# Kernel optimization log

Hardware: AMD Instinct MI355X
Metric: run time of the kernel (lower is better)

Reference implementation:

```python
import jax, jax.numpy as jnp
import numpy as np

N_DIM = 32
N_HEADS = 4
HEAD_SIZE = N_DIM // N_HEADS  # 8


def setup_inputs() -> dict:
    key = jax.random.key(0)
    ks = jax.random.split(key, 9)
    B, T = 16, 2048
    s = 1.0 / np.sqrt(N_DIM)
    inp = {
        "x": jax.random.normal(ks[0], (B, T, N_DIM), dtype=jnp.float32),
        "Wq": jax.random.uniform(ks[1], (N_DIM, N_DIM), jnp.float32, -s, s),
        "bq": jax.random.uniform(ks[2], (N_DIM,), jnp.float32, -s, s),
        "Wk": jax.random.uniform(ks[3], (N_DIM, N_DIM), jnp.float32, -s, s),
        "bk": jax.random.uniform(ks[4], (N_DIM,), jnp.float32, -s, s),
        "Wv": jax.random.uniform(ks[5], (N_DIM, N_DIM), jnp.float32, -s, s),
        "bv": jax.random.uniform(ks[6], (N_DIM,), jnp.float32, -s, s),
        "Wp": jax.random.uniform(ks[7], (N_DIM, N_DIM), jnp.float32, -s, s),
        "bp": jax.random.uniform(ks[8], (N_DIM,), jnp.float32, -s, s),
    }
    return inp


def reference(x, Wq, bq, Wk, bk, Wv, bv, Wp, bp):
    b, t, c = x.shape
    # nn.Linear: y = x @ W^T + b
    def heads(W, bias):
        y = jnp.einsum("btc,dc->btd", x, W) + bias
        return y.reshape(b, t, N_HEADS, HEAD_SIZE).transpose(0, 2, 1, 3)  # [b,h,t,d]

    q = heads(Wq, bq)
    k = heads(Wk, bk)
    v = heads(Wv, bv)

    scores = jnp.einsum("bhqd,bhkd->bhqk", q, k) / np.sqrt(HEAD_SIZE)  # [b,h,t,t]
    causal = jnp.tril(jnp.ones((t, t), dtype=bool))
    scores = jnp.where(causal[None, None], scores, -jnp.inf)
    weights = jax.nn.softmax(scores, axis=-1)
    # dropout layers are identity in eval mode
    z = jnp.einsum("bhqk,bhkd->bhqd", weights, v)
    z = z.transpose(0, 2, 1, 3).reshape(b, t, N_DIM)
    z = jnp.einsum("btc,dc->btd", z, Wp) + bp
    return z
```

## Files before the change

### kernel.cpp

```cpp
#include <hip/hip_runtime.h>
#include <math.h>

#define BB 16
#define TT 2048
#define CC 32
#define HH 4
#define DD 8

typedef __fp16 h2  __attribute__((ext_vector_type(2)));
typedef __fp16 h8  __attribute__((ext_vector_type(8)));
typedef float  fx16 __attribute__((ext_vector_type(16)));
typedef int    i4v __attribute__((ext_vector_type(4)));

__device__ __forceinline__ h2 pkh(float a, float b) {
#if __has_builtin(__builtin_amdgcn_cvt_pkrtz)
    return __builtin_amdgcn_cvt_pkrtz(a, b);
#else
    h2 r; r.x = (__fp16)a; r.y = (__fp16)b; return r;
#endif
}

__device__ __forceinline__ float fexp2(float x) {
#if __has_builtin(__builtin_amdgcn_exp2f)
    return __builtin_amdgcn_exp2f(x);
#else
    return exp2f(x);
#endif
}

__device__ __forceinline__ int h2bits(h2 v) { return __builtin_bit_cast(int, v); }

__global__ __launch_bounds__(256) void qkv_kernel(
    const float* __restrict__ x,
    const float* __restrict__ Wq, const float* __restrict__ bq,
    const float* __restrict__ Wk, const float* __restrict__ bk,
    const float* __restrict__ Wv, const float* __restrict__ bv,
    __fp16* __restrict__ Qo, __fp16* __restrict__ Ko, __fp16* __restrict__ Vo)
{
    const int row = blockIdx.x * 256 + threadIdx.x;
    const int m = blockIdx.y >> 2, h = blockIdx.y & 3;
    const int b = row >> 11, t = row & 2047;
    const int bh = b * HH + h;

    const float* W    = (m == 0) ? Wq : (m == 1) ? Wk : Wv;
    const float* bias = (m == 0) ? bq : (m == 1) ? bk : bv;

    float xr[CC];
    const float4* xp = (const float4*)(x + (size_t)row * CC);
    #pragma unroll
    for (int i = 0; i < CC / 4; i++) {
        float4 f = xp[i];
        xr[4*i+0] = f.x; xr[4*i+1] = f.y; xr[4*i+2] = f.z; xr[4*i+3] = f.w;
    }

    float o[DD];
    #pragma unroll
    for (int d = 0; d < DD; d++) {
        const int dd = h * DD + d;
        float acc = bias[dd];
        #pragma unroll
        for (int c = 0; c < CC; c++) acc += xr[c] * W[dd * CC + c];
        o[d] = acc;
    }

    if (m == 0) {
        const float qs = 0.3535533905932738f * 1.4426950408889634f;
        i4v qw;
        qw.x = h2bits(pkh(o[0]*qs, o[1]*qs)); qw.y = h2bits(pkh(o[2]*qs, o[3]*qs));
        qw.z = h2bits(pkh(o[4]*qs, o[5]*qs)); qw.w = h2bits(pkh(o[6]*qs, o[7]*qs));
        *(i4v*)(Qo + ((size_t)bh * TT + t) * DD) = qw;
    } else if (m == 1) {
        i4v kw;
        kw.x = h2bits(pkh(o[0], o[1])); kw.y = h2bits(pkh(o[2], o[3]));
        kw.z = h2bits(pkh(o[4], o[5])); kw.w = h2bits(pkh(o[6], o[7]));
        *(i4v*)(Ko + ((size_t)bh * TT + t) * DD) = kw;
    } else {
        __fp16* vt = Vo + (size_t)bh * 9 * TT + t;
        #pragma unroll
        for (int d = 0; d < DD; d++) vt[d * TT] = (__fp16)o[d];
        vt[8 * TT] = (__fp16)1.0f;
    }
}

__global__ __launch_bounds__(512, 4) void attn_kernel(
    const __fp16* __restrict__ Qg, const __fp16* __restrict__ Kg,
    const __fp16* __restrict__ Vg, float* __restrict__ Z)
{
    __shared__ __align__(16) __fp16 Ks[TT * DD + 8];
    __shared__ __align__(16) __fp16 Vts[9 * TT];

    const int tid  = threadIdx.x;
    const int bh   = blockIdx.x >> 3;
    const int bi   = blockIdx.x & 7;
    const int wave = tid >> 6;
    const int lane = tid & 63;
    const int qc   = lane & 31;
    const int hi   = lane >> 5;

    {
        const i4v* Ksrc = (const i4v*)(Kg + (size_t)bh * TT * DD);
        i4v* Kd = (i4v*)Ks;
        for (int i = tid; i < TT * DD / 8; i += 512) Kd[i] = Ksrc[i];
        const i4v* Vsrc = (const i4v*)(Vg + (size_t)bh * 9 * TT);
        i4v* Vd = (i4v*)Vts;
        for (int i = tid; i < 9 * TT / 8; i += 512) Vd[i] = Vsrc[i];
        if (tid == 0) {
            i4v zz; zz.x = 0; zz.y = 0; zz.z = 0; zz.w = 0;
            Kd[TT * DD / 8] = zz;
        }
    }
    __syncthreads();

    const int j = (wave + bi) & 7;
    const int g = 16 * (j >> 1) + ((j & 1) ? (15 - bi) : bi);
    const int qbase = g * 32;
    const int q = qbase + qc;

    h8 qf;
    {
        h8 ql = *(const h8*)(Qg + ((size_t)bh * TT + q) * DD);
        h8 qz;
        #pragma unroll
        for (int i = 0; i < 8; i++) qz[i] = (__fp16)0.0f;
        qf = hi ? qz : ql;
    }

    fx16 O, zc;
    #pragma unroll
    for (int i = 0; i < 16; i++) { O[i] = 0.0f; zc[i] = 0.0f; }

    const int vrow = (qc < 9) ? qc : 8;
    const __fp16* vbase = Vts + vrow * TT + 8 * hi;
    const __fp16* kptr  = Ks + qc * DD;
    const int thr = qc - 4 * hi;

    for (int kt = 0; kt <= qbase; kt += 32) {
        const bool last = (kt == qbase);

        h8 kf = *(const h8*)(kptr + kt * DD);
        fx16 S = __builtin_amdgcn_mfma_f32_32x32x16_f16(kf, qf, zc, 0, 0, 0);

        float p[16];
        #pragma unroll
        for (int r = 0; r < 16; r++) {
            const int ko = (r & 3) + 8 * (r >> 2);
            float sv = S[r];
            if (last) sv = (ko <= thr) ? sv : -INFINITY;
            p[r] = fexp2(sv);
        }

        int Hh[8];
        #pragma unroll
        for (int i = 0; i < 8; i++) Hh[i] = h2bits(pkh(p[2*i], p[2*i+1]));

        #pragma unroll
        for (int s = 0; s < 2; s++) {
            const int b0 = 4 * s;
            int own0 = hi ? Hh[b0+2] : Hh[b0+0];
            int own1 = hi ? Hh[b0+3] : Hh[b0+1];
            int snd0 = hi ? Hh[b0+0] : Hh[b0+2];
            int snd1 = hi ? Hh[b0+1] : Hh[b0+3];
            int rcv0 = __shfl_xor(snd0, 32);
            int rcv1 = __shfl_xor(snd1, 32);
            i4v f;
            f.x = hi ? rcv0 : own0;
            f.y = hi ? rcv1 : own1;
            f.z = hi ? own0 : rcv0;
            f.w = hi ? own1 : rcv1;
            h8 P = __builtin_bit_cast(h8, f);
            h8 vf = *(const h8*)(vbase + kt + 16 * s);
            O = __builtin_amdgcn_mfma_f32_32x32x16_f16(vf, P, O, 0, 0, 0);
        }
    }

    const float inv = 1.0f / O[4];
    const int b = bh >> 2, h = bh & 3;
    float* z = Z + ((size_t)b * TT + q) * CC + h * DD + 4 * hi;
    *(float4*)z = make_float4(O[0]*inv, O[1]*inv, O[2]*inv, O[3]*inv);
}

__global__ __launch_bounds__(256) void proj_kernel(
    const float* __restrict__ Zw, const float* __restrict__ Wp,
    const float* __restrict__ bp, float* __restrict__ out)
{
    const int row = blockIdx.x * 256 + threadIdx.x;
    const int oc = blockIdx.y;

    float zr[CC];
    const float4* zp = (const float4*)(Zw + (size_t)row * CC);
    #pragma unroll
    for (int i = 0; i < CC / 4; i++) {
        float4 f = zp[i];
        zr[4*i+0] = f.x; zr[4*i+1] = f.y; zr[4*i+2] = f.z; zr[4*i+3] = f.w;
    }

    float o[DD];
    #pragma unroll
    for (int d = 0; d < DD; d++) {
        const int dd = oc * DD + d;
        float acc = bp[dd];
        #pragma unroll
        for (int c = 0; c < CC; c++) acc += zr[c] * Wp[dd * CC + c];
        o[d] = acc;
    }

    float* dst = out + (size_t)row * CC + oc * DD;
    ((float4*)dst)[0] = make_float4(o[0], o[1], o[2], o[3]);
    ((float4*)dst)[1] = make_float4(o[4], o[5], o[6], o[7]);
}

extern "C" void kernel_launch(void* const* d_in, const int* in_sizes, int n_in,
                              void* d_out, int out_size, void* d_ws, size_t ws_size,
                              hipStream_t stream) {
    const float* x  = (const float*)d_in[0];
    const float* Wq = (const float*)d_in[1];
    const float* bq = (const float*)d_in[2];
    const float* Wk = (const float*)d_in[3];
    const float* bk = (const float*)d_in[4];
    const float* Wv = (const float*)d_in[5];
    const float* bv = (const float*)d_in[6];
    const float* Wp = (const float*)d_in[7];
    const float* bp = (const float*)d_in[8];
    float* out = (float*)d_out;

    const size_t NE = (size_t)BB * HH * TT * DD;
    __fp16* Qh = (__fp16*)d_ws;
    __fp16* Kh = Qh + NE;
    __fp16* Vt = Kh + NE;
    float*  Zw = (float*)(Vt + (size_t)BB * HH * 9 * TT);

    qkv_kernel<<<dim3(BB * TT / 256, 12), 256, 0, stream>>>(x, Wq, bq, Wk, bk, Wv, bv, Qh, Kh, Vt);
    attn_kernel<<<dim3(BB * HH * 8), 512, 0, stream>>>(Qh, Kh, Vt, Zw);
    proj_kernel<<<dim3(BB * TT / 256, 4), 256, 0, stream>>>(Zw, Wp, bp, out);
}
```

Before: 119.7 us.

## Fuse output projection into attention and restructure blocks across heads with streamed K/V tiles

The attention kernel now assigns each block 64 query rows of one batch across all four heads. It streams K/V in 256-key chunks through padded shared memory instead of loading each head's full K/V. The output projection is fused in through a shared-memory Z buffer, which removes the separate proj kernel and the Z round trip through global memory. The QKV kernel stages x through shared memory and loops over heads per block, which cuts redundant x reads. In exchange there are many more __syncthreads, and waves idle through chunks beyond their causal range. Load imbalance across blocks also changes.

Result: slower. 130.0 us (+8.6%).

```diff
diff --git a/kernel.cpp b/kernel.cpp
--- a/kernel.cpp
+++ b/kernel.cpp
@@ -6,6 +6,11 @@
 #define CC 32
 #define HH 4
 #define DD 8
+
+#define KP 2056
+#define VP 264
+#define VHP (9 * VP)
+#define ZP 33
 
 typedef __fp16 h2  __attribute__((ext_vector_type(2)));
 typedef __fp16 h8  __attribute__((ext_vector_type(8)));
@@ -37,84 +42,88 @@
     const float* __restrict__ Wv, const float* __restrict__ bv,
     __fp16* __restrict__ Qo, __fp16* __restrict__ Ko, __fp16* __restrict__ Vo)
 {
-    const int row = blockIdx.x * 256 + threadIdx.x;
-    const int m = blockIdx.y >> 2, h = blockIdx.y & 3;
+    __shared__ float Xs[256 * ZP];
+    const int tid = threadIdx.x;
+    const int m = blockIdx.y;
+    const int row0 = blockIdx.x * 256;
+
+    {
+        const float4* xg = (const float4*)(x + (size_t)row0 * CC);
+        #pragma unroll
+        for (int i = 0; i < 8; i++) {
+            const int idx = tid + 256 * i;
+            float4 f = xg[idx];
+            const int w = idx * 4;
+            float* d = &Xs[(w >> 5) * ZP + (w & 31)];
+            d[0] = f.x; d[1] = f.y; d[2] = f.z; d[3] = f.w;
+        }
+    }
+    __syncthreads();
+
+    const int row = row0 + tid;
     const int b = row >> 11, t = row & 2047;
-    const int bh = b * HH + h;
+
+    float xr[CC];
+    #pragma unroll
+    for (int c = 0; c < CC; c++) xr[c] = Xs[tid * ZP + c];
 
     const float* W    = (m == 0) ? Wq : (m == 1) ? Wk : Wv;
     const float* bias = (m == 0) ? bq : (m == 1) ? bk : bv;
 
-    float xr[CC];
-    const float4* xp = (const float4*)(x + (size_t)row * CC);
-    #pragma unroll
-    for (int i = 0; i < CC / 4; i++) {
-        float4 f = xp[i];
-        xr[4*i+0] = f.x; xr[4*i+1] = f.y; xr[4*i+2] = f.z; xr[4*i+3] = f.w;
-    }
-
-    float o[DD];
-    #pragma unroll
-    for (int d = 0; d < DD; d++) {
-        const int dd = h * DD + d;
-        float acc = bias[dd];
-        #pragma unroll
-        for (int c = 0; c < CC; c++) acc += xr[c] * W[dd * CC + c];
-        o[d] = acc;
-    }
-
-    if (m == 0) {
-        const float qs = 0.3535533905932738f * 1.4426950408889634f;
-        i4v qw;
-        qw.x = h2bits(pkh(o[0]*qs, o[1]*qs)); qw.y = h2bits(pkh(o[2]*qs, o[3]*qs));
-        qw.z = h2bits(pkh(o[4]*qs, o[5]*qs)); qw.w = h2bits(pkh(o[6]*qs, o[7]*qs));
-        *(i4v*)(Qo + ((size_t)bh * TT + t) * DD) = qw;
-    } else if (m == 1) {
-        i4v kw;
-        kw.x = h2bits(pkh(o[0], o[1])); kw.y = h2bits(pkh(o[2], o[3]));
-        kw.z = h2bits(pkh(o[4], o[5])); kw.w = h2bits(pkh(o[6], o[7]));
-        *(i4v*)(Ko + ((size_t)bh * TT + t) * DD) = kw;
-    } else {
-        __fp16* vt = Vo + (size_t)bh * 9 * TT + t;
-        #pragma unroll
-        for (int d = 0; d < DD; d++) vt[d * TT] = (__fp16)o[d];
-        vt[8 * TT] = (__fp16)1.0f;
+    for (int h = 0; h < HH; h++) {
+        const int bh = b * HH + h;
+        float o[DD];
+        #pragma unroll
+        for (int d = 0; d < DD; d++) {
+            const int dd = h * DD + d;
+            float acc = bias[dd];
+            #pragma unroll
+            for (int c = 0; c < CC; c++) acc += xr[c] * W[dd * CC + c];
+            o[d] = acc;
+        }
+        if (m == 0) {
+            const float qs = 0.3535533905932738f * 1.4426950408889634f;
+            i4v qw;
+            qw.x = h2bits(pkh(o[0]*qs, o[1]*qs)); qw.y = h2bits(pkh(o[2]*qs, o[3]*qs));
+            qw.z = h2bits(pkh(o[4]*qs, o[5]*qs)); qw.w = h2bits(pkh(o[6]*qs, o[7]*qs));
+            *(i4v*)(Qo + ((size_t)bh * TT + t) * DD) = qw;
+        } else if (m == 1) {
+            i4v kw;
+            kw.x = h2bits(pkh(o[0], o[1])); kw.y = h2bits(pkh(o[2], o[3]));
+            kw.z = h2bits(pkh(o[4], o[5])); kw.w = h2bits(pkh(o[6], o[7]));
+            *(i4v*)(Ko + ((size_t)bh * TT + t) * DD) = kw;
+        } else {
+            __fp16* vt = Vo + (size_t)bh * 9 * TT + t;
+            #pragma unroll
+            for (int d = 0; d < DD; d++) vt[d * TT] = (__fp16)o[d];
+            vt[8 * TT] = (__fp16)1.0f;
+        }
     }
 }
 
 __global__ __launch_bounds__(512, 4) void attn_kernel(
     const __fp16* __restrict__ Qg, const __fp16* __restrict__ Kg,
-    const __fp16* __restrict__ Vg, float* __restrict__ Z)
+    const __fp16* __restrict__ Vg,
+    const float* __restrict__ Wp, const float* __restrict__ bp,
+    float* __restrict__ out)
 {
-    __shared__ __align__(16) __fp16 Ks[TT * DD + 8];
-    __shared__ __align__(16) __fp16 Vts[9 * TT];
-
-    const int tid  = threadIdx.x;
-    const int bh   = blockIdx.x >> 3;
-    const int bi   = blockIdx.x & 7;
-    const int wave = tid >> 6;
-    const int lane = tid & 63;
-    const int qc   = lane & 31;
-    const int hi   = lane >> 5;
-
-    {
-        const i4v* Ksrc = (const i4v*)(Kg + (size_t)bh * TT * DD);
-        i4v* Kd = (i4v*)Ks;
-        for (int i = tid; i < TT * DD / 8; i += 512) Kd[i] = Ksrc[i];
-        const i4v* Vsrc = (const i4v*)(Vg + (size_t)bh * 9 * TT);
-        i4v* Vd = (i4v*)Vts;
-        for (int i = tid; i < 9 * TT / 8; i += 512) Vd[i] = Vsrc[i];
-        if (tid == 0) {
-            i4v zz; zz.x = 0; zz.y = 0; zz.z = 0; zz.w = 0;
-            Kd[TT * DD / 8] = zz;
-        }
-    }
-    __syncthreads();
-
-    const int j = (wave + bi) & 7;
-    const int g = 16 * (j >> 1) + ((j & 1) ? (15 - bi) : bi);
-    const int qbase = g * 32;
-    const int q = qbase + qc;
+    __shared__ __align__(16) __fp16 KsS[4 * KP];
+    __shared__ __align__(16) __fp16 VtS[4 * VHP];
+    __shared__ float zbuf[64 * ZP];
+
+    const int tid   = threadIdx.x;
+    const int b     = blockIdx.x & 15;
+    const int qg    = 31 - (blockIdx.x >> 4);
+    const int wavei = tid >> 6;
+    const int lane  = tid & 63;
+    const int qc    = lane & 31;
+    const int hi    = lane >> 5;
+    const int h     = wavei & 3;
+    const int p     = wavei >> 2;
+
+    const int bh    = b * HH + h;
+    const int qbase = qg * 64 + p * 32;
+    const int q     = qbase + qc;
 
     h8 qf;
     {
@@ -130,83 +139,100 @@
     for (int i = 0; i < 16; i++) { O[i] = 0.0f; zc[i] = 0.0f; }
 
     const int vrow = (qc < 9) ? qc : 8;
-    const __fp16* vbase = Vts + vrow * TT + 8 * hi;
-    const __fp16* kptr  = Ks + qc * DD;
-    const int thr = qc - 4 * hi;
-
-    for (int kt = 0; kt <= qbase; kt += 32) {
-        const bool last = (kt == qbase);
-
-        h8 kf = *(const h8*)(kptr + kt * DD);
-        fx16 S = __builtin_amdgcn_mfma_f32_32x32x16_f16(kf, qf, zc, 0, 0, 0);
-
-        float p[16];
-        #pragma unroll
-        for (int r = 0; r < 16; r++) {
-            const int ko = (r & 3) + 8 * (r >> 2);
-            float sv = S[r];
-            if (last) sv = (ko <= thr) ? sv : -INFINITY;
-            p[r] = fexp2(sv);
-        }
-
-        int Hh[8];
-        #pragma unroll
-        for (int i = 0; i < 8; i++) Hh[i] = h2bits(pkh(p[2*i], p[2*i+1]));
-
-        #pragma unroll
-        for (int s = 0; s < 2; s++) {
-            const int b0 = 4 * s;
-            int own0 = hi ? Hh[b0+2] : Hh[b0+0];
-            int own1 = hi ? Hh[b0+3] : Hh[b0+1];
-            int snd0 = hi ? Hh[b0+0] : Hh[b0+2];
-            int snd1 = hi ? Hh[b0+1] : Hh[b0+3];
-            int rcv0 = __shfl_xor(snd0, 32);
-            int rcv1 = __shfl_xor(snd1, 32);
-            i4v f;
-            f.x = hi ? rcv0 : own0;
-            f.y = hi ? rcv1 : own1;
-            f.z = hi ? own0 : rcv0;
-            f.w = hi ? own1 : rcv1;
-            h8 P = __builtin_bit_cast(h8, f);
-            h8 vf = *(const h8*)(vbase + kt + 16 * s);
-            O = __builtin_amdgcn_mfma_f32_32x32x16_f16(vf, P, O, 0, 0, 0);
-        }
-    }
-
-    const float inv = 1.0f / O[4];
-    const int b = bh >> 2, h = bh & 3;
-    float* z = Z + ((size_t)b * TT + q) * CC + h * DD + 4 * hi;
-    *(float4*)z = make_float4(O[0]*inv, O[1]*inv, O[2]*inv, O[3]*inv);
-}
-
-__global__ __launch_bounds__(256) void proj_kernel(
-    const float* __restrict__ Zw, const float* __restrict__ Wp,
-    const float* __restrict__ bp, float* __restrict__ out)
-{
-    const int row = blockIdx.x * 256 + threadIdx.x;
-    const int oc = blockIdx.y;
-
-    float zr[CC];
-    const float4* zp = (const float4*)(Zw + (size_t)row * CC);
-    #pragma unroll
-    for (int i = 0; i < CC / 4; i++) {
-        float4 f = zp[i];
-        zr[4*i+0] = f.x; zr[4*i+1] = f.y; zr[4*i+2] = f.z; zr[4*i+3] = f.w;
-    }
-
-    float o[DD];
-    #pragma unroll
-    for (int d = 0; d < DD; d++) {
-        const int dd = oc * DD + d;
-        float acc = bp[dd];
-        #pragma unroll
-        for (int c = 0; c < CC; c++) acc += zr[c] * Wp[dd * CC + c];
-        o[d] = acc;
-    }
-
-    float* dst = out + (size_t)row * CC + oc * DD;
-    ((float4*)dst)[0] = make_float4(o[0], o[1], o[2], o[3]);
-    ((float4*)dst)[1] = make_float4(o[4], o[5], o[6], o[7]);
+    const int thr  = qc - 4 * hi;
+    const int nst  = qg / 4 + 1;
+
+    for (int sti = 0; sti < nst; sti++) {
+        const int st = sti * 256;
+        __syncthreads();
+        {
+            const int hh = tid >> 7, tl = tid & 127;
+            const i4v* ks = (const i4v*)(Kg + ((size_t)(b * HH + hh) * TT + st) * DD);
+            i4v* kd = (i4v*)(KsS + hh * KP);
+            kd[tl]       = ks[tl];
+            kd[tl + 128] = ks[tl + 128];
+            #pragma unroll
+            for (int i0 = 0; i0 < 3; i0++) {
+                const int i = tl + 128 * i0;
+                if (i < 288) {
+                    const int vr = i >> 5, vc = (i & 31) * 8;
+                    *(i4v*)(VtS + hh * VHP + vr * VP + vc) =
+                        *(const i4v*)(Vg + ((size_t)(b * HH + hh) * 9 + vr) * TT + st + vc);
+                }
+            }
+        }
+        __syncthreads();
+
+        if (st > qbase) continue;
+        const int ktend = min(st + 256, qbase + 32);
+        const __fp16* kbase = KsS + h * KP + qc * DD;
+        const __fp16* vb    = VtS + h * VHP + vrow * VP + 8 * hi;
+
+        for (int kt = st; kt < ktend; kt += 32) {
+            const bool last = (kt == qbase);
+
+            h8 kf = *(const h8*)(kbase + (kt - st) * DD);
+            fx16 S = __builtin_amdgcn_mfma_f32_32x32x16_f16(kf, qf, zc, 0, 0, 0);
+
+            float pe[16];
+            #pragma unroll
+            for (int r = 0; r < 16; r++) {
+                const int ko = (r & 3) + 8 * (r >> 2);
+                float sv = S[r];
+                if (last) sv = (ko <= thr) ? sv : -INFINITY;
+                pe[r] = fexp2(sv);
+            }
+
+            int Hh[8];
+            #pragma unroll
+            for (int i = 0; i < 8; i++) Hh[i] = h2bits(pkh(pe[2*i], pe[2*i+1]));
+
+            #pragma unroll
+            for (int s = 0; s < 2; s++) {
+                const int b0 = 4 * s;
+                int own0 = hi ? Hh[b0+2] : Hh[b0+0];
+                int own1 = hi ? Hh[b0+3] : Hh[b0+1];
+                int snd0 = hi ? Hh[b0+0] : Hh[b0+2];
+                int snd1 = hi ? Hh[b0+1] : Hh[b0+3];
+                int rcv0 = __shfl_xor(snd0, 32);
+                int rcv1 = __shfl_xor(snd1, 32);
+                i4v f;
+                f.x = hi ? rcv0 : own0;
+                f.y = hi ? rcv1 : own1;
+                f.z = hi ? own0 : rcv0;
+                f.w = hi ? own1 : rcv1;
+                h8 P = __builtin_bit_cast(h8, f);
+                h8 vf = *(const h8*)(vb + (kt - st) + 16 * s);
+                O = __builtin_amdgcn_mfma_f32_32x32x16_f16(vf, P, O, 0, 0, 0);
+            }
+        }
+    }
+
+    {
+        const float inv = 1.0f / O[4];
+        float* zp_ = &zbuf[(p * 32 + qc) * ZP + h * DD + 4 * hi];
+        zp_[0] = O[0]*inv; zp_[1] = O[1]*inv; zp_[2] = O[2]*inv; zp_[3] = O[3]*inv;
+    }
+    __syncthreads();
+
+    {
+        const int seg = wavei;
+        const int r = lane;
+        float zr_[CC];
+        #pragma unroll
+        for (int c = 0; c < CC; c++) zr_[c] = zbuf[r * ZP + c];
+        float o4[4];
+        #pragma unroll
+        for (int d = 0; d < 4; d++) {
+            const int dd = seg * 4 + d;
+            float acc = bp[dd];
+            #pragma unroll
+            for (int c = 0; c < CC; c++) acc += zr_[c] * Wp[dd * CC + c];
+            o4[d] = acc;
+        }
+        float* dst = out + ((size_t)b * TT + qg * 64 + r) * CC + seg * 4;
+        *(float4*)dst = make_float4(o4[0], o4[1], o4[2], o4[3]);
+    }
 }
 
 extern "C" void kernel_launch(void* const* d_in, const int* in_sizes, int n_in,
@@ -227,9 +253,7 @@
     __fp16* Qh = (__fp16*)d_ws;
     __fp16* Kh = Qh + NE;
     __fp16* Vt = Kh + NE;
-    float*  Zw = (float*)(Vt + (size_t)BB * HH * 9 * TT);
-
-    qkv_kernel<<<dim3(BB * TT / 256, 12), 256, 0, stream>>>(x, Wq, bq, Wk, bk, Wv, bv, Qh, Kh, Vt);
-    attn_kernel<<<dim3(BB * HH * 8), 512, 0, stream>>>(Qh, Kh, Vt, Zw);
-    proj_kernel<<<dim3(BB * TT / 256, 4), 256, 0, stream>>>(Zw, Wp, bp, out);
-}
+
+    qkv_kernel<<<dim3(BB * TT / 256, 3), 256, 0, stream>>>(x, Wq, bq, Wk, bk, Wv, bv, Qh, Kh, Vt);
+    attn_kernel<<<dim3(BB * 32), 512, 0, stream>>>(Qh, Kh, Vt, Wp, bp, out);
+}
```

## Split attention into single-wave blocks streaming K/V chunks; loop heads in QKV

Applied to the files above, without the earlier changes.

The attention kernel now launches one 64-thread block per (query tile, batch-head) pair, 4096 blocks in all, instead of 512-thread blocks that each staged a whole head's K and V in LDS. Each block streams K/V in 256-key chunks through small LDS buffers and orders tiles so the longest causal work is scheduled first. The aim is to cut LDS footprint, raise occupancy and balance load, at the cost of re-reading K/V from global memory once per query tile. The QKV kernel stages x through padded shared memory and loops over the four heads inside each block, reading x once per matrix rather than once per head.

New measurement: 130.4 us. +9.0%, slower.

```diff
diff --git a/kernel.cpp b/kernel.cpp
--- a/kernel.cpp
+++ b/kernel.cpp
@@ -6,6 +6,9 @@
 #define CC 32
 #define HH 4
 #define DD 8
+#define ZP 33
+#define KBS 2056
+#define VRS 264
 
 typedef __fp16 h2  __attribute__((ext_vector_type(2)));
 typedef __fp16 h8  __attribute__((ext_vector_type(8)));
@@ -29,6 +32,36 @@
 }
 
 __device__ __forceinline__ int h2bits(h2 v) { return __builtin_bit_cast(int, v); }
+
+__device__ __forceinline__ void makeP(const fx16& S, bool last, int thr, int hi, h8* P) {
+    float pe[16];
+    #pragma unroll
+    for (int r = 0; r < 16; r++) {
+        const int ko = (r & 3) + 8 * (r >> 2);
+        float sv = S[r];
+        if (last) sv = (ko <= thr) ? sv : -INFINITY;
+        pe[r] = fexp2(sv);
+    }
+    int Hh[8];
+    #pragma unroll
+    for (int i = 0; i < 8; i++) Hh[i] = h2bits(pkh(pe[2*i], pe[2*i+1]));
+    #pragma unroll
+    for (int s = 0; s < 2; s++) {
+        const int b0 = 4 * s;
+        int own0 = hi ? Hh[b0+2] : Hh[b0+0];
+        int own1 = hi ? Hh[b0+3] : Hh[b0+1];
+        int snd0 = hi ? Hh[b0+0] : Hh[b0+2];
+        int snd1 = hi ? Hh[b0+1] : Hh[b0+3];
+        int rcv0 = __shfl_xor(snd0, 32);
+        int rcv1 = __shfl_xor(snd1, 32);
+        i4v f;
+        f.x = hi ? rcv0 : own0;
+        f.y = hi ? rcv1 : own1;
+        f.z = hi ? own0 : rcv0;
+        f.w = hi ? own1 : rcv1;
+        P[s] = __builtin_bit_cast(h8, f);
+    }
+}
 
 __global__ __launch_bounds__(256) void qkv_kernel(
     const float* __restrict__ x,
@@ -37,91 +70,91 @@
     const float* __restrict__ Wv, const float* __restrict__ bv,
     __fp16* __restrict__ Qo, __fp16* __restrict__ Ko, __fp16* __restrict__ Vo)
 {
-    const int row = blockIdx.x * 256 + threadIdx.x;
-    const int m = blockIdx.y >> 2, h = blockIdx.y & 3;
+    __shared__ float Xs[256 * ZP];
+    const int tid = threadIdx.x;
+    const int m = blockIdx.y;
+    const int row0 = blockIdx.x * 256;
+
+    {
+        const float4* xg = (const float4*)(x + (size_t)row0 * CC);
+        #pragma unroll
+        for (int i = 0; i < 8; i++) {
+            const int idx = tid + 256 * i;
+            float4 f = xg[idx];
+            const int w = idx * 4;
+            float* d = &Xs[(w >> 5) * ZP + (w & 31)];
+            d[0] = f.x; d[1] = f.y; d[2] = f.z; d[3] = f.w;
+        }
+    }
+    __syncthreads();
+
+    const int row = row0 + tid;
     const int b = row >> 11, t = row & 2047;
-    const int bh = b * HH + h;
+
+    float xr[CC];
+    #pragma unroll
+    for (int c = 0; c < CC; c++) xr[c] = Xs[tid * ZP + c];
 
     const float* W    = (m == 0) ? Wq : (m == 1) ? Wk : Wv;
     const float* bias = (m == 0) ? bq : (m == 1) ? bk : bv;
 
-    float xr[CC];
-    const float4* xp = (const float4*)(x + (size_t)row * CC);
-    #pragma unroll
-    for (int i = 0; i < CC / 4; i++) {
-        float4 f = xp[i];
-        xr[4*i+0] = f.x; xr[4*i+1] = f.y; xr[4*i+2] = f.z; xr[4*i+3] = f.w;
-    }
-
-    float o[DD];
-    #pragma unroll
-    for (int d = 0; d < DD; d++) {
-        const int dd = h * DD + d;
-        float acc = bias[dd];
-        #pragma unroll
-        for (int c = 0; c < CC; c++) acc += xr[c] * W[dd * CC + c];
-        o[d] = acc;
-    }
-
-    if (m == 0) {
-        const float qs = 0.3535533905932738f * 1.4426950408889634f;
-        i4v qw;
-        qw.x = h2bits(pkh(o[0]*qs, o[1]*qs)); qw.y = h2bits(pkh(o[2]*qs, o[3]*qs));
-        qw.z = h2bits(pkh(o[4]*qs, o[5]*qs)); qw.w = h2bits(pkh(o[6]*qs, o[7]*qs));
-        *(i4v*)(Qo + ((size_t)bh * TT + t) * DD) = qw;
-    } else if (m == 1) {
-        i4v kw;
-        kw.x = h2bits(pkh(o[0], o[1])); kw.y = h2bits(pkh(o[2], o[3]));
-        kw.z = h2bits(pkh(o[4], o[5])); kw.w = h2bits(pkh(o[6], o[7]));
-        *(i4v*)(Ko + ((size_t)bh * TT + t) * DD) = kw;
-    } else {
-        __fp16* vt = Vo + (size_t)bh * 9 * TT + t;
-        #pragma unroll
-        for (int d = 0; d < DD; d++) vt[d * TT] = (__fp16)o[d];
-        vt[8 * TT] = (__fp16)1.0f;
-    }
-}
-
-__global__ __launch_bounds__(512, 4) void attn_kernel(
+    for (int h = 0; h < HH; h++) {
+        const int bh = b * HH + h;
+        float o[DD];
+        #pragma unroll
+        for (int d = 0; d < DD; d++) {
+            const int dd = h * DD + d;
+            float acc = bias[dd];
+            #pragma unroll
+            for (int c = 0; c < CC; c++) acc += xr[c] * W[dd * CC + c];
+            o[d] = acc;
+        }
+        if (m == 0) {
+            const float qs = 0.3535533905932738f * 1.4426950408889634f;
+            i4v qw;
+            qw.x = h2bits(pkh(o[0]*qs, o[1]*qs)); qw.y = h2bits(pkh(o[2]*qs, o[3]*qs));
+            qw.z = h2bits(pkh(o[4]*qs, o[5]*qs)); qw.w = h2bits(pkh(o[6]*qs, o[7]*qs));
+            *(i4v*)(Qo + ((size_t)bh * TT + t) * DD) = qw;
+        } else if (m == 1) {
+            i4v kw;
+            kw.x = h2bits(pkh(o[0], o[1])); kw.y = h2bits(pkh(o[2], o[3]));
+            kw.z = h2bits(pkh(o[4], o[5])); kw.w = h2bits(pkh(o[6], o[7]));
+            *(i4v*)(Ko + ((size_t)bh * TT + t) * DD) = kw;
+        } else {
+            __fp16* vt = Vo + (size_t)bh * 9 * TT + t;
+            #pragma unroll
+            for (int d = 0; d < DD; d++) vt[d * TT] = (__fp16)o[d];
+            vt[8 * TT] = (__fp16)1.0f;
+        }
+    }
+}
+
+__global__ __launch_bounds__(64, 4) void attn_kernel(
     const __fp16* __restrict__ Qg, const __fp16* __restrict__ Kg,
-    const __fp16* __restrict__ Vg, float* __restrict__ Z)
+    const __fp16* __restrict__ Vg, float* __restrict__ Zw)
 {
-    __shared__ __align__(16) __fp16 Ks[TT * DD + 8];
-    __shared__ __align__(16) __fp16 Vts[9 * TT];
-
-    const int tid  = threadIdx.x;
-    const int bh   = blockIdx.x >> 3;
-    const int bi   = blockIdx.x & 7;
-    const int wave = tid >> 6;
-    const int lane = tid & 63;
+    __shared__ __align__(16) __fp16 kld[KBS];
+    __shared__ __align__(16) __fp16 vld[9 * VRS];
+
+    const int bid  = blockIdx.x;
+    const int t    = bid >> 6;
+    const int bh   = bid & 63;
+    const int r_   = t >> 4, c_ = t & 15;
+    const int g    = (r_ == 0) ? (63 - c_) : (r_ == 1) ? c_ : (r_ == 2) ? (47 - c_) : (16 + c_);
+
+    const int lane = threadIdx.x;
     const int qc   = lane & 31;
     const int hi   = lane >> 5;
 
-    {
-        const i4v* Ksrc = (const i4v*)(Kg + (size_t)bh * TT * DD);
-        i4v* Kd = (i4v*)Ks;
-        for (int i = tid; i < TT * DD / 8; i += 512) Kd[i] = Ksrc[i];
-        const i4v* Vsrc = (const i4v*)(Vg + (size_t)bh * 9 * TT);
-        i4v* Vd = (i4v*)Vts;
-        for (int i = tid; i < 9 * TT / 8; i += 512) Vd[i] = Vsrc[i];
-        if (tid == 0) {
-            i4v zz; zz.x = 0; zz.y = 0; zz.z = 0; zz.w = 0;
-            Kd[TT * DD / 8] = zz;
-        }
-    }
-    __syncthreads();
-
-    const int j = (wave + bi) & 7;
-    const int g = 16 * (j >> 1) + ((j & 1) ? (15 - bi) : bi);
-    const int qbase = g * 32;
-    const int q = qbase + qc;
+    const int qbase = 32 * g;
+    const int q     = qbase + qc;
 
     h8 qf;
     {
+        h8 qz;
+        #pragma unroll
+        for (int i = 0; i < 8; i++) qz[i] = (__fp16)0.0f;
         h8 ql = *(const h8*)(Qg + ((size_t)bh * TT + q) * DD);
-        h8 qz;
-        #pragma unroll
-        for (int i = 0; i < 8; i++) qz[i] = (__fp16)0.0f;
         qf = hi ? qz : ql;
     }
 
@@ -130,52 +163,48 @@
     for (int i = 0; i < 16; i++) { O[i] = 0.0f; zc[i] = 0.0f; }
 
     const int vrow = (qc < 9) ? qc : 8;
-    const __fp16* vbase = Vts + vrow * TT + 8 * hi;
-    const __fp16* kptr  = Ks + qc * DD;
-    const int thr = qc - 4 * hi;
-
-    for (int kt = 0; kt <= qbase; kt += 32) {
-        const bool last = (kt == qbase);
-
-        h8 kf = *(const h8*)(kptr + kt * DD);
-        fx16 S = __builtin_amdgcn_mfma_f32_32x32x16_f16(kf, qf, zc, 0, 0, 0);
-
-        float p[16];
-        #pragma unroll
-        for (int r = 0; r < 16; r++) {
-            const int ko = (r & 3) + 8 * (r >> 2);
-            float sv = S[r];
-            if (last) sv = (ko <= thr) ? sv : -INFINITY;
-            p[r] = fexp2(sv);
-        }
-
-        int Hh[8];
-        #pragma unroll
-        for (int i = 0; i < 8; i++) Hh[i] = h2bits(pkh(p[2*i], p[2*i+1]));
-
-        #pragma unroll
-        for (int s = 0; s < 2; s++) {
-            const int b0 = 4 * s;
-            int own0 = hi ? Hh[b0+2] : Hh[b0+0];
-            int own1 = hi ? Hh[b0+3] : Hh[b0+1];
-            int snd0 = hi ? Hh[b0+0] : Hh[b0+2];
-            int snd1 = hi ? Hh[b0+1] : Hh[b0+3];
-            int rcv0 = __shfl_xor(snd0, 32);
-            int rcv1 = __shfl_xor(snd1, 32);
-            i4v f;
-            f.x = hi ? rcv0 : own0;
-            f.y = hi ? rcv1 : own1;
-            f.z = hi ? own0 : rcv0;
-            f.w = hi ? own1 : rcv1;
-            h8 P = __builtin_bit_cast(h8, f);
-            h8 vf = *(const h8*)(vbase + kt + 16 * s);
-            O = __builtin_amdgcn_mfma_f32_32x32x16_f16(vf, P, O, 0, 0, 0);
+    const int thr  = qc - 4 * hi;
+
+    const __fp16* kgl = Kg + (size_t)bh * TT * DD;
+    const __fp16* vgl = Vg + (size_t)bh * 9 * TT;
+    const __fp16* kb  = kld + qc * DD;
+    const __fp16* vb  = vld + vrow * VRS + 8 * hi;
+
+    const int keys = qbase + 32;
+    for (int st = 0; st < keys; st += 256) {
+        __syncthreads();
+        {
+            const i4v* ks = (const i4v*)(kgl + (size_t)st * DD);
+            i4v* kd = (i4v*)kld;
+            #pragma unroll
+            for (int r = 0; r < 4; r++) kd[lane + 64 * r] = ks[lane + 64 * r];
+            #pragma unroll
+            for (int r = 0; r < 5; r++) {
+                const int i = lane + 64 * r;
+                if (i < 288)
+                    *(i4v*)(vld + (i >> 5) * VRS + (i & 31) * 8) =
+                        *(const i4v*)(vgl + (i >> 5) * TT + st + (i & 31) * 8);
+            }
+        }
+        __syncthreads();
+
+        const int kend = min(st + 256, keys);
+        for (int kt = st; kt < kend; kt += 32) {
+            h8 kf = *(const h8*)(kb + (kt - st) * DD);
+            fx16 S = __builtin_amdgcn_mfma_f32_32x32x16_f16(kf, qf, zc, 0, 0, 0);
+            h8 P[2];
+            makeP(S, kt == qbase, thr, hi, P);
+            #pragma unroll
+            for (int s = 0; s < 2; s++) {
+                h8 vf = *(const h8*)(vb + (kt - st) + 16 * s);
+                O = __builtin_amdgcn_mfma_f32_32x32x16_f16(vf, P[s], O, 0, 0, 0);
+            }
         }
     }
 
     const float inv = 1.0f / O[4];
     const int b = bh >> 2, h = bh & 3;
-    float* z = Z + ((size_t)b * TT + q) * CC + h * DD + 4 * hi;
+    float* z = Zw + ((size_t)b * TT + q) * CC + h * DD + 4 * hi;
     *(float4*)z = make_float4(O[0]*inv, O[1]*inv, O[2]*inv, O[3]*inv);
 }
 
@@ -229,7 +258,7 @@
     __fp16* Vt = Kh + NE;
     float*  Zw = (float*)(Vt + (size_t)BB * HH * 9 * TT);
 
-    qkv_kernel<<<dim3(BB * TT / 256, 12), 256, 0, stream>>>(x, Wq, bq, Wk, bk, Wv, bv, Qh, Kh, Vt);
-    attn_kernel<<<dim3(BB * HH * 8), 512, 0, stream>>>(Qh, Kh, Vt, Zw);
+    qkv_kernel<<<dim3(BB * TT / 256, 3), 256, 0, stream>>>(x, Wq, bq, Wk, bk, Wv, bv, Qh, Kh, Vt);
+    attn_kernel<<<dim3(64 * 64), 64, 0, stream>>>(Qh, Kh, Vt, Zw);
     proj_kernel<<<dim3(BB * TT / 256, 4), 256, 0, stream>>>(Zw, Wp, bp, out);
 }
```
